# Optimization experiments

Measured on AMD Instinct MI355X. Metric: run time of the kernel, lower is better.

The kernel has to match this reference:

```python
import jax, jax.numpy as jnp
import numpy as np

N = 50000      # nodes
E = 1600000    # edges (avg degree 32)
D_IN = 128
H = 256        # 2 * out_channels
D_OUT = 128
NEG_SLOPE = 0.2


def setup_inputs() -> dict:
    key = jax.random.key(0)
    ks = jax.random.split(key, 16)
    x = jax.random.normal(ks[0], (N, D_IN), dtype=jnp.float32)
    edge_index = jax.random.randint(ks[1], (2, E), 0, N, dtype=jnp.int64)

    def lin(k, fan_in, fan_out):
        s = 1.0 / np.sqrt(fan_in)
        return jax.random.uniform(k, (fan_in, fan_out), jnp.float32, -s, s)

    def att(k, d):
        s = 1.0 / np.sqrt(d)
        return jax.random.uniform(k, (d,), jnp.float32, -s, s)

    return {
        "x": x, "edge_index": edge_index,
        "W1": lin(ks[2], D_IN, H), "a1_src": att(ks[3], H), "a1_dst": att(ks[4], H), "b1": jnp.zeros((H,), jnp.float32),
        "W2": lin(ks[5], H, H),    "a2_src": att(ks[6], H), "a2_dst": att(ks[7], H), "b2": jnp.zeros((H,), jnp.float32),
        "W3": lin(ks[8], H, D_OUT),"a3_src": att(ks[9], D_OUT), "a3_dst": att(ks[10], D_OUT), "b3": jnp.zeros((D_OUT,), jnp.float32),
    }


def _gat_conv(x, W, a_src, a_dst, b, src, dst):
    # x: [N, Cin] -> h: [N, Cout]
    h = x @ W
    # per-node attention logits, gathered along edges (edge j->i: src=j, dst=i)
    e = jax.nn.leaky_relu((h @ a_src)[src] + (h @ a_dst)[dst], NEG_SLOPE)  # [E]
    # segment softmax over incoming edges of each destination node
    m = jax.ops.segment_max(e, dst, num_segments=N)          # [N]
    p = jnp.exp(e - m[dst])                                  # [E]
    denom = jax.ops.segment_sum(p, dst, num_segments=N)      # [N]
    alpha = p / denom[dst]                                   # [E]
    # scatter-add weighted source features
    out = jax.ops.segment_sum(alpha[:, None] * h[src], dst, num_segments=N)
    return out + b


def reference(x, edge_index, W1, a1_src, a1_dst, b1, W2, a2_src, a2_dst, b2, W3, a3_src, a3_dst, b3):
    src, dst = edge_index[0], edge_index[1]
    h = jax.nn.relu(_gat_conv(x, W1, a1_src, a1_dst, b1, src, dst))
    for _ in range(2):  # hidden_layers, shared conv2 weights
        h = jax.nn.relu(_gat_conv(h, W2, a2_src, a2_dst, b2, src, dst))
    out = _gat_conv(h, W3, a3_src, a3_dst, b3, src, dst)
    return jax.nn.softmax(out, axis=1)
```

## Files before the change

kernel.cpp:

```cpp
#include <hip/hip_runtime.h>
#include <hip/hip_bf16.h>
#include <hip/hip_fp16.h>

#define NN 50000
#define EE 1600000
#define DIN 128
#define HH 256
#define DOUT 128

typedef __attribute__((ext_vector_type(8))) short short8;
typedef __attribute__((ext_vector_type(4))) float f32x4;

__device__ __forceinline__ short f2bf(float v) {
    union { float f; unsigned u; } a;
    a.f = v;
    unsigned r = a.u + 0x7fffu + ((a.u >> 16) & 1u);
    return (short)(r >> 16);
}
__device__ __forceinline__ float bf2f(short h) {
    union { unsigned u; float f; } a;
    a.u = ((unsigned)(unsigned short)h) << 16;
    return a.f;
}


__global__ __launch_bounds__(256) void hist_kernel(const int* __restrict__ dst, int* __restrict__ deg, int E) {
    int e = blockIdx.x * 256 + threadIdx.x;
    if (e < E) atomicAdd(&deg[dst[e]], 1);
}

#define SCAN_B 256

__global__ __launch_bounds__(SCAN_B) void scan1_kernel(const int* __restrict__ deg, int* __restrict__ exc,
                                                       int* __restrict__ bsum, int n) {
    __shared__ int tmp[SCAN_B];
    int i = blockIdx.x * SCAN_B + threadIdx.x;
    int v = (i < n) ? deg[i] : 0;
    tmp[threadIdx.x] = v;
    __syncthreads();
    for (int o = 1; o < SCAN_B; o <<= 1) {
        int t = (threadIdx.x >= o) ? tmp[threadIdx.x - o] : 0;
        __syncthreads();
        tmp[threadIdx.x] += t;
        __syncthreads();
    }
    if (i < n) exc[i] = tmp[threadIdx.x] - v;
    if (threadIdx.x == SCAN_B - 1) bsum[blockIdx.x] = tmp[SCAN_B - 1];
}

__global__ __launch_bounds__(SCAN_B) void scan2_kernel(int* __restrict__ bsum, int nb) {
    __shared__ int tmp[SCAN_B];
    int v = (threadIdx.x < nb) ? bsum[threadIdx.x] : 0;
    tmp[threadIdx.x] = v;
    __syncthreads();
    for (int o = 1; o < SCAN_B; o <<= 1) {
        int t = (threadIdx.x >= o) ? tmp[threadIdx.x - o] : 0;
        __syncthreads();
        tmp[threadIdx.x] += t;
        __syncthreads();
    }
    if (threadIdx.x < nb) bsum[threadIdx.x] = tmp[threadIdx.x] - v;
}

__global__ __launch_bounds__(SCAN_B) void scan3_kernel(int* __restrict__ exc, const int* __restrict__ bsum,
                                                       int* __restrict__ cursor, int n, int E) {
    int i = blockIdx.x * SCAN_B + threadIdx.x;
    if (i < n) {
        int v = exc[i] + bsum[blockIdx.x];
        exc[i] = v;
        cursor[i] = v;
    }
    if (i == n) exc[n] = E;
}

__global__ __launch_bounds__(256) void scatter_kernel(const int* __restrict__ src, const int* __restrict__ dst,
                                                      int* __restrict__ cursor, int* __restrict__ es, int E) {
    int e = blockIdx.x * 256 + threadIdx.x;
    if (e < E) {
        int d = dst[e];
        int pos = atomicAdd(&cursor[d], 1);
        es[pos] = src[e];
    }
}


__global__ __launch_bounds__(256) void wsplit_kernel(const float* __restrict__ W, short* __restrict__ WhT,
                                                     short* __restrict__ WlT, int K, int C) {
    int f = blockIdx.x * 256 + threadIdx.x;
    if (f >= K * C) return;
    int k = f / C, c = f % C;
    float v = W[f];
    short h = f2bf(v);
    short l = f2bf(v - bf2f(h));
    WhT[(size_t)c * K + k] = h;
    WlT[(size_t)c * K + k] = l;
}


__global__ __launch_bounds__(256) void tohalf_kernel(const float* __restrict__ in, __half* __restrict__ out,
                                                     size_t cnt) {
    size_t i = (size_t)(blockIdx.x * 256 + threadIdx.x) * 4;
    if (i + 3 < cnt) {
        float4 v = *(const float4*)(in + i);
        __half h0 = __float2half(v.x), h1 = __float2half(v.y);
        __half h2 = __float2half(v.z), h3 = __float2half(v.w);
        __half2* op = (__half2*)(out + i);
        op[0] = __half2(h0, h1);
        op[1] = __half2(h2, h3);
    }
}


template <bool BRELU, bool DOTS, bool HOUT>
__global__ __launch_bounds__(256) void gemm_mfma_kernel(const float* __restrict__ X, const short* __restrict__ BhT,
                                                        const short* __restrict__ BlT, const float* __restrict__ bias,
                                                        float* __restrict__ out, const float* __restrict__ a1v,
                                                        const float* __restrict__ a2v, float* __restrict__ s1,
                                                        float* __restrict__ s2, int n, int K, int Cout) {
    __shared__ short Ah[128][40], Al[128][40];
    __shared__ short Bh[128][40], Bl[128][40];
    int tid = threadIdx.x;
    int row0 = blockIdx.y * 128, col0 = blockIdx.x * 128;
    int lane = tid & 63, wid = tid >> 6;
    int wr = (wid >> 1) * 64, wc = (wid & 1) * 64;

    f32x4 acc[4][4];
#pragma unroll
    for (int mi = 0; mi < 4; ++mi)
#pragma unroll
        for (int ni = 0; ni < 4; ++ni) acc[mi][ni] = 0.f;

    int srow = tid >> 1;
    int sk = (tid & 1) * 16;

    for (int k0 = 0; k0 < K; k0 += 32) {
        {
            float v[16];
            int gr = row0 + srow;
            if (gr < n) {
                const float* p = X + (size_t)gr * K + k0 + sk;
                float4 f0 = ((const float4*)p)[0];
                float4 f1 = ((const float4*)p)[1];
                float4 f2 = ((const float4*)p)[2];
                float4 f3 = ((const float4*)p)[3];
                v[0] = f0.x; v[1] = f0.y; v[2] = f0.z; v[3] = f0.w;
                v[4] = f1.x; v[5] = f1.y; v[6] = f1.z; v[7] = f1.w;
                v[8] = f2.x; v[9] = f2.y; v[10] = f2.z; v[11] = f2.w;
                v[12] = f3.x; v[13] = f3.y; v[14] = f3.z; v[15] = f3.w;
            } else {
#pragma unroll
                for (int j = 0; j < 16; ++j) v[j] = 0.f;
            }
            short8 h0, h1, l0, l1;
#pragma unroll
            for (int j = 0; j < 8; ++j) {
                short h = f2bf(v[j]);
                h0[j] = h;
                l0[j] = f2bf(v[j] - bf2f(h));
            }
#pragma unroll
            for (int j = 0; j < 8; ++j) {
                short h = f2bf(v[8 + j]);
                h1[j] = h;
                l1[j] = f2bf(v[8 + j] - bf2f(h));
            }
            *(short8*)&Ah[srow][sk] = h0;
            *(short8*)&Ah[srow][sk + 8] = h1;
            *(short8*)&Al[srow][sk] = l0;
            *(short8*)&Al[srow][sk + 8] = l1;
        }
        {
            const short* ph = BhT + (size_t)(col0 + srow) * K + k0 + sk;
            const short* pl = BlT + (size_t)(col0 + srow) * K + k0 + sk;
            short8 bh0 = ((const short8*)ph)[0];
            short8 bh1 = ((const short8*)ph)[1];
            short8 bl0 = ((const short8*)pl)[0];
            short8 bl1 = ((const short8*)pl)[1];
            *(short8*)&Bh[srow][sk] = bh0;
            *(short8*)&Bh[srow][sk + 8] = bh1;
            *(short8*)&Bl[srow][sk] = bl0;
            *(short8*)&Bl[srow][sk + 8] = bl1;
        }
        __syncthreads();

        int fr = lane & 15, kb = lane >> 4;
        short8 a_h[4], a_l[4];
#pragma unroll
        for (int mi = 0; mi < 4; ++mi) {
            a_h[mi] = *(const short8*)&Ah[wr + mi * 16 + fr][kb * 8];
            a_l[mi] = *(const short8*)&Al[wr + mi * 16 + fr][kb * 8];
        }
#pragma unroll
        for (int ni = 0; ni < 4; ++ni) {
            short8 b_h = *(const short8*)&Bh[wc + ni * 16 + fr][kb * 8];
            short8 b_l = *(const short8*)&Bl[wc + ni * 16 + fr][kb * 8];
#pragma unroll
            for (int mi = 0; mi < 4; ++mi) {
                acc[mi][ni] = __builtin_amdgcn_mfma_f32_16x16x32_bf16(a_l[mi], b_h, acc[mi][ni], 0, 0, 0);
                acc[mi][ni] = __builtin_amdgcn_mfma_f32_16x16x32_bf16(a_h[mi], b_l, acc[mi][ni], 0, 0, 0);
                acc[mi][ni] = __builtin_amdgcn_mfma_f32_16x16x32_bf16(a_h[mi], b_h, acc[mi][ni], 0, 0, 0);
            }
        }
        __syncthreads();
    }

    int dc = lane & 15, dr = (lane >> 4) * 4;

    if (DOTS) {
#pragma unroll
        for (int mi = 0; mi < 4; ++mi) {
#pragma unroll
            for (int r = 0; r < 4; ++r) {
                float p1 = 0.f, p2 = 0.f;
#pragma unroll
                for (int ni = 0; ni < 4; ++ni) {
                    int gcol = col0 + wc + ni * 16 + dc;
                    float v = acc[mi][ni][r];
                    p1 = fmaf(v, a1v[gcol], p1);
                    p2 = fmaf(v, a2v[gcol], p2);
                }
#pragma unroll
                for (int o = 8; o; o >>= 1) {
                    p1 += __shfl_xor(p1, o, 64);
                    p2 += __shfl_xor(p2, o, 64);
                }
                int grow = row0 + wr + mi * 16 + dr + r;
                if (dc == 0 && grow < n) {
                    atomicAdd(s1 + grow, p1);
                    atomicAdd(s2 + grow, p2);
                }
            }
        }
    }

#pragma unroll
    for (int mi = 0; mi < 4; ++mi) {
#pragma unroll
        for (int r = 0; r < 4; ++r) {
            int grow = row0 + wr + mi * 16 + dr + r;
            if (grow >= n) continue;
#pragma unroll
            for (int ni = 0; ni < 4; ++ni) {
                int gcol = col0 + wc + ni * 16 + dc;
                float v = acc[mi][ni][r];
                if (BRELU) {
                    v += bias[gcol];
                    v = fmaxf(v, 0.f);
                }
                if (HOUT) {
                    ((__half*)out)[(size_t)grow * Cout + gcol] = __float2half(v);
                } else {
                    out[(size_t)grow * Cout + gcol] = v;
                }
            }
        }
    }
}


__global__ __launch_bounds__(256) void rowdots_kernel(const float* __restrict__ H, const float* __restrict__ a1,
                                                      const float* __restrict__ a2, float* __restrict__ s1,
                                                      float* __restrict__ s2, int n, int C) {
    int w = (blockIdx.x * 256 + threadIdx.x) >> 6;
    int lane = threadIdx.x & 63;
    if (w >= n) return;
    const float* hp = H + (size_t)w * C;
    float acc1 = 0.f, acc2 = 0.f;
    for (int c = lane; c < C; c += 64) {
        float hv = hp[c];
        acc1 = fmaf(hv, a1[c], acc1);
        acc2 = fmaf(hv, a2[c], acc2);
    }
#pragma unroll
    for (int o = 32; o; o >>= 1) {
        acc1 += __shfl_xor(acc1, o, 64);
        acc2 += __shfl_xor(acc2, o, 64);
    }
    if (lane == 0) {
        s1[w] = acc1;
        s2[w] = acc2;
    }
}


__global__ __launch_bounds__(256) void mden_kernel(const float* __restrict__ ssrc, const float* __restrict__ sdst,
                                                   const int* __restrict__ off, const int* __restrict__ esrc,
                                                   float* __restrict__ alpha, float* __restrict__ invden, int n) {
    int w = (blockIdx.x * 256 + threadIdx.x) >> 6;
    int lane = threadIdx.x & 63;
    if (w >= n) return;
    int beg = off[w], end = off[w + 1];
    float sd = sdst[w];
    float m = -3e38f;
    for (int e = beg + lane; e < end; e += 64) {
        float v = ssrc[esrc[e]] + sd;
        v = (v > 0.f) ? v : 0.2f * v;
        alpha[e] = v;
        m = fmaxf(m, v);
    }
#pragma unroll
    for (int o = 32; o; o >>= 1) m = fmaxf(m, __shfl_xor(m, o, 64));
    float den = 0.f;
    for (int e = beg + lane; e < end; e += 64) {
        float p = __expf(alpha[e] - m);
        alpha[e] = p;
        den += p;
    }
#pragma unroll
    for (int o = 32; o; o >>= 1) den += __shfl_xor(den, o, 64);
    if (lane == 0) invden[w] = (den > 0.f) ? 1.f / den : 0.f;
}


template <int C, bool RELU, bool SOFTMAX>
__global__ __launch_bounds__(256) void aggc2_kernel(const __half* __restrict__ H, const float* __restrict__ alpha,
                                                    const float* __restrict__ invden, const int* __restrict__ off,
                                                    const int* __restrict__ esrc, const float* __restrict__ bias,
                                                    float* __restrict__ out, int n) {
    constexpr int WPN = C / 128;
    constexpr int NPB = 4 / WPN;
    int wid = threadIdx.x >> 6, lane = threadIdx.x & 63;
    int node = blockIdx.x * NPB + (WPN == 1 ? wid : (wid >> 1));
    int wv = (WPN == 1) ? 0 : (wid & 1);
    int c0 = wv * 128 + lane * 2;
    int beg = (node < n) ? off[node] : 0;
    int end = (node < n) ? off[node + 1] : 0;

    float acc0 = 0.f, acc1 = 0.f;
    for (int base = beg; base < end; base += 64) {
        int e = base + lane;
        float pl = 0.f;
        int sl = 0;
        if (e < end) {
            pl = alpha[e];
            sl = esrc[e];
        }
        int cnt = end - base;
        if (cnt > 64) cnt = 64;
        int j0 = 0;
        for (; j0 + 8 <= cnt; j0 += 8) {
            float pj[8];
            const __half2* hp[8];
#pragma unroll
            for (int u = 0; u < 8; ++u) {
                pj[u] = __shfl(pl, j0 + u, 64);
                int sj = __shfl(sl, j0 + u, 64);
                hp[u] = (const __half2*)(H + (size_t)sj * C + c0);
            }
            __half2 hv[8];
#pragma unroll
            for (int u = 0; u < 8; ++u) hv[u] = *hp[u];
#pragma unroll
            for (int u = 0; u < 8; ++u) {
                float2 f = __half22float2(hv[u]);
                acc0 = fmaf(pj[u], f.x, acc0);
                acc1 = fmaf(pj[u], f.y, acc1);
            }
        }
        for (; j0 < cnt; ++j0) {
            float pj = __shfl(pl, j0, 64);
            int sj = __shfl(sl, j0, 64);
            float2 f = __half22float2(*(const __half2*)(H + (size_t)sj * C + c0));
            acc0 = fmaf(pj, f.x, acc0);
            acc1 = fmaf(pj, f.y, acc1);
        }
    }

    float ov0 = 0.f, ov1 = 0.f;
    if (node < n) {
        float inv = invden[node];
        float bb0 = bias ? bias[c0] : 0.f;
        float bb1 = bias ? bias[c0 + 1] : 0.f;
        ov0 = fmaf(acc0, inv, bb0);
        ov1 = fmaf(acc1, inv, bb1);
        if (RELU) {
            ov0 = fmaxf(ov0, 0.f);
            ov1 = fmaxf(ov1, 0.f);
        }
    }
    if (SOFTMAX) {
        float mm = fmaxf(ov0, ov1);
#pragma unroll
        for (int o = 32; o; o >>= 1) mm = fmaxf(mm, __shfl_xor(mm, o, 64));
        float e0 = __expf(ov0 - mm), e1 = __expf(ov1 - mm);
        float ss = e0 + e1;
#pragma unroll
        for (int o = 32; o; o >>= 1) ss += __shfl_xor(ss, o, 64);
        float si = 1.f / ss;
        ov0 = e0 * si;
        ov1 = e1 * si;
    }
    if (node < n) *(float2*)(out + (size_t)node * C + c0) = make_float2(ov0, ov1);
}


extern "C" void kernel_launch(void* const* d_in, const int* in_sizes, int n_in,
                              void* d_out, int out_size, void* d_ws, size_t ws_size,
                              hipStream_t stream) {
    const float* x = (const float*)d_in[0];
    const int* ei = (const int*)d_in[1];
    const float* W1 = (const float*)d_in[2];
    const float* a1s = (const float*)d_in[3];
    const float* a1d = (const float*)d_in[4];
    const float* b1 = (const float*)d_in[5];
    const float* W2 = (const float*)d_in[6];
    const float* a2s = (const float*)d_in[7];
    const float* a2d = (const float*)d_in[8];
    const float* b2 = (const float*)d_in[9];
    const float* W3 = (const float*)d_in[10];
    const float* a3s = (const float*)d_in[11];
    const float* a3d = (const float*)d_in[12];
    const float* b3 = (const float*)d_in[13];

    const int n = NN, E = EE;
    const int* src = ei;
    const int* dst = ei + E;

    char* base = (char*)d_ws;
    size_t o = 0;
    auto alloc = [&](size_t bytes) -> char* {
        char* p = base + o;
        o += (bytes + 255) & ~(size_t)255;
        return p;
    };
    int* off = (int*)alloc((n + 1) * sizeof(int));
    int* cur = (int*)alloc((n + 1) * sizeof(int));
    int* bsum = (int*)alloc(1024 * sizeof(int));
    int* es = (int*)alloc((size_t)E * sizeof(int));
    float* sbuf = (float*)alloc((size_t)2 * n * sizeof(float));
    float* ssrc = sbuf;
    float* sdst = sbuf + n;
    float* alpha = (float*)alloc((size_t)E * sizeof(float));
    float* invden = (float*)alloc((size_t)n * sizeof(float));
    float* was = (float*)alloc(256 * sizeof(float));
    float* wad = (float*)alloc(256 * sizeof(float));
    short* W1h = (short*)alloc((size_t)DIN * HH * sizeof(short));
    short* W1l = (short*)alloc((size_t)DIN * HH * sizeof(short));
    short* W2h = (short*)alloc((size_t)HH * HH * sizeof(short));
    short* W2l = (short*)alloc((size_t)HH * HH * sizeof(short));
    short* W3h = (short*)alloc((size_t)HH * DOUT * sizeof(short));
    short* W3l = (short*)alloc((size_t)HH * DOUT * sizeof(short));
    __half* xh = (__half*)alloc((size_t)n * DIN * sizeof(__half));
    __half* Hh = (__half*)alloc((size_t)n * HH * sizeof(__half));
    float* Hbuf = (float*)alloc((size_t)n * HH * sizeof(float));
    float* Abuf = (float*)alloc((size_t)n * HH * sizeof(float));
    (void)ws_size;

    hipMemsetAsync(cur, 0, (n + 1) * sizeof(int), stream);
    hist_kernel<<<(E + 255) / 256, 256, 0, stream>>>(dst, cur, E);
    int nb = (n + SCAN_B - 1) / SCAN_B;
    scan1_kernel<<<nb, SCAN_B, 0, stream>>>(cur, off, bsum, n);
    scan2_kernel<<<1, SCAN_B, 0, stream>>>(bsum, nb);
    scan3_kernel<<<nb, SCAN_B, 0, stream>>>(off, bsum, cur, n, E);
    scatter_kernel<<<(E + 255) / 256, 256, 0, stream>>>(src, dst, cur, es, E);

    wsplit_kernel<<<(DIN * HH + 255) / 256, 256, 0, stream>>>(W1, W1h, W1l, DIN, HH);
    wsplit_kernel<<<(HH * HH + 255) / 256, 256, 0, stream>>>(W2, W2h, W2l, HH, HH);
    wsplit_kernel<<<(HH * DOUT + 255) / 256, 256, 0, stream>>>(W3, W3h, W3l, HH, DOUT);
    tohalf_kernel<<<((n * DIN / 4) + 255) / 256, 256, 0, stream>>>(x, xh, (size_t)n * DIN);

    int wgrid = (n * 64 + 255) / 256;
    int rb = (n + 127) / 128;

    {
        rowdots_kernel<<<(128 * 64 + 255) / 256, 256, 0, stream>>>(W1, a1s, a1d, was, wad, DIN, HH);
        rowdots_kernel<<<wgrid, 256, 0, stream>>>(x, was, wad, ssrc, sdst, n, DIN);
        mden_kernel<<<wgrid, 256, 0, stream>>>(ssrc, sdst, off, es, alpha, invden, n);
        aggc2_kernel<DIN, false, false><<<n / 4, 256, 0, stream>>>(xh, alpha, invden, off, es, nullptr, Hbuf, n);
        dim3 g(HH / 128, rb);
        gemm_mfma_kernel<true, false, false><<<g, 256, 0, stream>>>(Hbuf, W1h, W1l, b1, Abuf, nullptr, nullptr,
                                                                    nullptr, nullptr, n, DIN, HH);
    }
    for (int t = 0; t < 2; ++t) {
        dim3 g(HH / 128, rb);
        hipMemsetAsync(sbuf, 0, (size_t)2 * n * sizeof(float), stream);
        gemm_mfma_kernel<false, true, true><<<g, 256, 0, stream>>>(Abuf, W2h, W2l, nullptr, (float*)Hh, a2s, a2d,
                                                                   ssrc, sdst, n, HH, HH);
        mden_kernel<<<wgrid, 256, 0, stream>>>(ssrc, sdst, off, es, alpha, invden, n);
        aggc2_kernel<HH, true, false><<<n / 2, 256, 0, stream>>>(Hh, alpha, invden, off, es, b2, Abuf, n);
    }
    {
        dim3 g(DOUT / 128, rb);
        hipMemsetAsync(sbuf, 0, (size_t)2 * n * sizeof(float), stream);
        gemm_mfma_kernel<false, true, true><<<g, 256, 0, stream>>>(Abuf, W3h, W3l, nullptr, (float*)Hh, a3s, a3d,
                                                                   ssrc, sdst, n, HH, DOUT);
        mden_kernel<<<wgrid, 256, 0, stream>>>(ssrc, sdst, off, es, alpha, invden, n);
        aggc2_kernel<DOUT, false, true><<<n / 4, 256, 0, stream>>>(Hh, alpha, invden, off, es, b3, (float*)d_out, n);
    }
}
```

Measured before the change: 760.7 us.

## Fuse softmax normalization into aggregation and partition CSR scatter by destination range

Removes the separate mden kernel and alpha/invden buffers. The aggregation kernel now recomputes edge logits, takes a per-node max, and computes exp weights and the denominator on the fly while gathering features. It also uses one wave per node with 4 channels per lane for C=256. The CSR scatter is split into 8 destination-range passes over edge chunks to localize atomics and writes, at the cost of reading dst eight times and gathering ssrc twice per edge.

```diff
diff --git a/kernel.cpp b/kernel.cpp
--- a/kernel.cpp
+++ b/kernel.cpp
@@ -73,13 +73,22 @@
     if (i == n) exc[n] = E;
 }
 
-__global__ __launch_bounds__(256) void scatter_kernel(const int* __restrict__ src, const int* __restrict__ dst,
-                                                      int* __restrict__ cursor, int* __restrict__ es, int E) {
-    int e = blockIdx.x * 256 + threadIdx.x;
-    if (e < E) {
+#define NCB 256
+
+__global__ __launch_bounds__(256) void scatter8_kernel(const int* __restrict__ src, const int* __restrict__ dst,
+                                                       int* __restrict__ cursor, int* __restrict__ es, int E, int n) {
+    int q = blockIdx.x & 7;
+    int cb = blockIdx.x >> 3;
+    int lo = q * (n >> 3);
+    int hi = (q == 7) ? n : lo + (n >> 3);
+    int chunk = (E + NCB - 1) / NCB;
+    int e1 = min((cb + 1) * chunk, E);
+    for (int e = cb * chunk + threadIdx.x; e < e1; e += 256) {
         int d = dst[e];
-        int pos = atomicAdd(&cursor[d], 1);
-        es[pos] = src[e];
+        if (d >= lo && d < hi) {
+            int pos = atomicAdd(&cursor[d], 1);
+            es[pos] = src[e];
+        }
     }
 }
 
@@ -283,114 +292,141 @@
 }
 
 
-__global__ __launch_bounds__(256) void mden_kernel(const float* __restrict__ ssrc, const float* __restrict__ sdst,
-                                                   const int* __restrict__ off, const int* __restrict__ esrc,
-                                                   float* __restrict__ alpha, float* __restrict__ invden, int n) {
-    int w = (blockIdx.x * 256 + threadIdx.x) >> 6;
-    int lane = threadIdx.x & 63;
-    if (w >= n) return;
-    int beg = off[w], end = off[w + 1];
-    float sd = sdst[w];
+template <int C, bool RELU, bool SOFTMAX>
+__global__ __launch_bounds__(256) void aggf_kernel(const __half* __restrict__ H, const float* __restrict__ ssrc,
+                                                   const float* __restrict__ sdst, const int* __restrict__ off,
+                                                   const int* __restrict__ es, const float* __restrict__ bias,
+                                                   float* __restrict__ out, int n) {
+    constexpr int VPL = C / 64;
+    int wid = threadIdx.x >> 6, lane = threadIdx.x & 63;
+    int node = blockIdx.x * 4 + wid;
+    if (node >= n) return;
+    int beg = off[node], end = off[node + 1];
+    float sd = sdst[node];
+
     float m = -3e38f;
     for (int e = beg + lane; e < end; e += 64) {
-        float v = ssrc[esrc[e]] + sd;
-        v = (v > 0.f) ? v : 0.2f * v;
-        alpha[e] = v;
-        m = fmaxf(m, v);
+        float g = ssrc[es[e]] + sd;
+        g = (g > 0.f) ? g : 0.2f * g;
+        m = fmaxf(m, g);
     }
 #pragma unroll
     for (int o = 32; o; o >>= 1) m = fmaxf(m, __shfl_xor(m, o, 64));
+
+    float acc[VPL];
+#pragma unroll
+    for (int v = 0; v < VPL; ++v) acc[v] = 0.f;
     float den = 0.f;
-    for (int e = beg + lane; e < end; e += 64) {
-        float p = __expf(alpha[e] - m);
-        alpha[e] = p;
-        den += p;
-    }
-#pragma unroll
-    for (int o = 32; o; o >>= 1) den += __shfl_xor(den, o, 64);
-    if (lane == 0) invden[w] = (den > 0.f) ? 1.f / den : 0.f;
-}
-
-
-template <int C, bool RELU, bool SOFTMAX>
-__global__ __launch_bounds__(256) void aggc2_kernel(const __half* __restrict__ H, const float* __restrict__ alpha,
-                                                    const float* __restrict__ invden, const int* __restrict__ off,
-                                                    const int* __restrict__ esrc, const float* __restrict__ bias,
-                                                    float* __restrict__ out, int n) {
-    constexpr int WPN = C / 128;
-    constexpr int NPB = 4 / WPN;
-    int wid = threadIdx.x >> 6, lane = threadIdx.x & 63;
-    int node = blockIdx.x * NPB + (WPN == 1 ? wid : (wid >> 1));
-    int wv = (WPN == 1) ? 0 : (wid & 1);
-    int c0 = wv * 128 + lane * 2;
-    int beg = (node < n) ? off[node] : 0;
-    int end = (node < n) ? off[node + 1] : 0;
-
-    float acc0 = 0.f, acc1 = 0.f;
+    int c0 = lane * VPL;
+
     for (int base = beg; base < end; base += 64) {
         int e = base + lane;
-        float pl = 0.f;
-        int sl = 0;
+        float p = 0.f;
+        int s = 0;
         if (e < end) {
-            pl = alpha[e];
-            sl = esrc[e];
+            s = es[e];
+            float g = ssrc[s] + sd;
+            g = (g > 0.f) ? g : 0.2f * g;
+            p = __expf(g - m);
+            den += p;
         }
         int cnt = end - base;
         if (cnt > 64) cnt = 64;
         int j0 = 0;
         for (; j0 + 8 <= cnt; j0 += 8) {
             float pj[8];
-            const __half2* hp[8];
+            const __half* hp[8];
 #pragma unroll
             for (int u = 0; u < 8; ++u) {
-                pj[u] = __shfl(pl, j0 + u, 64);
-                int sj = __shfl(sl, j0 + u, 64);
-                hp[u] = (const __half2*)(H + (size_t)sj * C + c0);
-            }
-            __half2 hv[8];
-#pragma unroll
-            for (int u = 0; u < 8; ++u) hv[u] = *hp[u];
-#pragma unroll
-            for (int u = 0; u < 8; ++u) {
-                float2 f = __half22float2(hv[u]);
-                acc0 = fmaf(pj[u], f.x, acc0);
-                acc1 = fmaf(pj[u], f.y, acc1);
+                pj[u] = __shfl(p, j0 + u, 64);
+                int sj = __shfl(s, j0 + u, 64);
+                hp[u] = H + (size_t)sj * C + c0;
+            }
+            if (VPL == 4) {
+                uint2 raw[8];
+#pragma unroll
+                for (int u = 0; u < 8; ++u) raw[u] = *(const uint2*)hp[u];
+#pragma unroll
+                for (int u = 0; u < 8; ++u) {
+                    union { unsigned u32; __half2 h2; } lo, hi;
+                    lo.u32 = raw[u].x;
+                    hi.u32 = raw[u].y;
+                    float2 f0 = __half22float2(lo.h2);
+                    float2 f1 = __half22float2(hi.h2);
+                    acc[0] = fmaf(pj[u], f0.x, acc[0]);
+                    acc[1] = fmaf(pj[u], f0.y, acc[1]);
+                    acc[2] = fmaf(pj[u], f1.x, acc[2]);
+                    acc[3] = fmaf(pj[u], f1.y, acc[3]);
+                }
+            } else {
+                __half2 hv[8];
+#pragma unroll
+                for (int u = 0; u < 8; ++u) hv[u] = *(const __half2*)hp[u];
+#pragma unroll
+                for (int u = 0; u < 8; ++u) {
+                    float2 f = __half22float2(hv[u]);
+                    acc[0] = fmaf(pj[u], f.x, acc[0]);
+                    acc[1] = fmaf(pj[u], f.y, acc[1]);
+                }
             }
         }
         for (; j0 < cnt; ++j0) {
-            float pj = __shfl(pl, j0, 64);
-            int sj = __shfl(sl, j0, 64);
-            float2 f = __half22float2(*(const __half2*)(H + (size_t)sj * C + c0));
-            acc0 = fmaf(pj, f.x, acc0);
-            acc1 = fmaf(pj, f.y, acc1);
-        }
-    }
-
-    float ov0 = 0.f, ov1 = 0.f;
-    if (node < n) {
-        float inv = invden[node];
-        float bb0 = bias ? bias[c0] : 0.f;
-        float bb1 = bias ? bias[c0 + 1] : 0.f;
-        ov0 = fmaf(acc0, inv, bb0);
-        ov1 = fmaf(acc1, inv, bb1);
-        if (RELU) {
-            ov0 = fmaxf(ov0, 0.f);
-            ov1 = fmaxf(ov1, 0.f);
-        }
+            float pj = __shfl(p, j0, 64);
+            int sj = __shfl(s, j0, 64);
+            const __half* hp = H + (size_t)sj * C + c0;
+            if (VPL == 4) {
+                uint2 raw = *(const uint2*)hp;
+                union { unsigned u32; __half2 h2; } lo, hi;
+                lo.u32 = raw.x;
+                hi.u32 = raw.y;
+                float2 f0 = __half22float2(lo.h2);
+                float2 f1 = __half22float2(hi.h2);
+                acc[0] = fmaf(pj, f0.x, acc[0]);
+                acc[1] = fmaf(pj, f0.y, acc[1]);
+                acc[2] = fmaf(pj, f1.x, acc[2]);
+                acc[3] = fmaf(pj, f1.y, acc[3]);
+            } else {
+                float2 f = __half22float2(*(const __half2*)hp);
+                acc[0] = fmaf(pj, f.x, acc[0]);
+                acc[1] = fmaf(pj, f.y, acc[1]);
+            }
+        }
+    }
+
+#pragma unroll
+    for (int o = 32; o; o >>= 1) den += __shfl_xor(den, o, 64);
+    float inv = (den > 0.f) ? 1.f / den : 0.f;
+
+    float ov[VPL];
+#pragma unroll
+    for (int v = 0; v < VPL; ++v) {
+        float bb = bias ? bias[c0 + v] : 0.f;
+        ov[v] = fmaf(acc[v], inv, bb);
+        if (RELU) ov[v] = fmaxf(ov[v], 0.f);
     }
     if (SOFTMAX) {
-        float mm = fmaxf(ov0, ov1);
+        float mm = ov[0];
+#pragma unroll
+        for (int v = 1; v < VPL; ++v) mm = fmaxf(mm, ov[v]);
 #pragma unroll
         for (int o = 32; o; o >>= 1) mm = fmaxf(mm, __shfl_xor(mm, o, 64));
-        float e0 = __expf(ov0 - mm), e1 = __expf(ov1 - mm);
-        float ss = e0 + e1;
+        float ss = 0.f;
+#pragma unroll
+        for (int v = 0; v < VPL; ++v) {
+            ov[v] = __expf(ov[v] - mm);
+            ss += ov[v];
+        }
 #pragma unroll
         for (int o = 32; o; o >>= 1) ss += __shfl_xor(ss, o, 64);
         float si = 1.f / ss;
-        ov0 = e0 * si;
-        ov1 = e1 * si;
-    }
-    if (node < n) *(float2*)(out + (size_t)node * C + c0) = make_float2(ov0, ov1);
+#pragma unroll
+        for (int v = 0; v < VPL; ++v) ov[v] *= si;
+    }
+    float* op = out + (size_t)node * C + c0;
+    if (VPL == 4)
+        *(float4*)op = make_float4(ov[0], ov[1], ov[2], ov[3]);
+    else
+        *(float2*)op = make_float2(ov[0], ov[1]);
 }
 
 
@@ -430,8 +466,6 @@
     float* sbuf = (float*)alloc((size_t)2 * n * sizeof(float));
     float* ssrc = sbuf;
     float* sdst = sbuf + n;
-    float* alpha = (float*)alloc((size_t)E * sizeof(float));
-    float* invden = (float*)alloc((size_t)n * sizeof(float));
     float* was = (float*)alloc(256 * sizeof(float));
     float* wad = (float*)alloc(256 * sizeof(float));
     short* W1h = (short*)alloc((size_t)DIN * HH * sizeof(short));
@@ -452,7 +486,7 @@
     scan1_kernel<<<nb, SCAN_B, 0, stream>>>(cur, off, bsum, n);
     scan2_kernel<<<1, SCAN_B, 0, stream>>>(bsum, nb);
     scan3_kernel<<<nb, SCAN_B, 0, stream>>>(off, bsum, cur, n, E);
-    scatter_kernel<<<(E + 255) / 256, 256, 0, stream>>>(src, dst, cur, es, E);
+    scatter8_kernel<<<NCB * 8, 256, 0, stream>>>(src, dst, cur, es, E, n);
 
     wsplit_kernel<<<(DIN * HH + 255) / 256, 256, 0, stream>>>(W1, W1h, W1l, DIN, HH);
     wsplit_kernel<<<(HH * HH + 255) / 256, 256, 0, stream>>>(W2, W2h, W2l, HH, HH);
@@ -460,13 +494,13 @@
     tohalf_kernel<<<((n * DIN / 4) + 255) / 256, 256, 0, stream>>>(x, xh, (size_t)n * DIN);
 
     int wgrid = (n * 64 + 255) / 256;
+    int agrid = (n + 3) / 4;
     int rb = (n + 127) / 128;
 
     {
         rowdots_kernel<<<(128 * 64 + 255) / 256, 256, 0, stream>>>(W1, a1s, a1d, was, wad, DIN, HH);
         rowdots_kernel<<<wgrid, 256, 0, stream>>>(x, was, wad, ssrc, sdst, n, DIN);
-        mden_kernel<<<wgrid, 256, 0, stream>>>(ssrc, sdst, off, es, alpha, invden, n);
-        aggc2_kernel<DIN, false, false><<<n / 4, 256, 0, stream>>>(xh, alpha, invden, off, es, nullptr, Hbuf, n);
+        aggf_kernel<DIN, false, false><<<agrid, 256, 0, stream>>>(xh, ssrc, sdst, off, es, nullptr, Hbuf, n);
         dim3 g(HH / 128, rb);
         gemm_mfma_kernel<true, false, false><<<g, 256, 0, stream>>>(Hbuf, W1h, W1l, b1, Abuf, nullptr, nullptr,
                                                                     nullptr, nullptr, n, DIN, HH);
@@ -476,15 +510,13 @@
         hipMemsetAsync(sbuf, 0, (size_t)2 * n * sizeof(float), stream);
         gemm_mfma_kernel<false, true, true><<<g, 256, 0, stream>>>(Abuf, W2h, W2l, nullptr, (float*)Hh, a2s, a2d,
                                                                    ssrc, sdst, n, HH, HH);
-        mden_kernel<<<wgrid, 256, 0, stream>>>(ssrc, sdst, off, es, alpha, invden, n);
-        aggc2_kernel<HH, true, false><<<n / 2, 256, 0, stream>>>(Hh, alpha, invden, off, es, b2, Abuf, n);
+        aggf_kernel<HH, true, false><<<agrid, 256, 0, stream>>>(Hh, ssrc, sdst, off, es, b2, Abuf, n);
     }
     {
         dim3 g(DOUT / 128, rb);
         hipMemsetAsync(sbuf, 0, (size_t)2 * n * sizeof(float), stream);
         gemm_mfma_kernel<false, true, true><<<g, 256, 0, stream>>>(Abuf, W3h, W3l, nullptr, (float*)Hh, a3s, a3d,
                                                                    ssrc, sdst, n, HH, DOUT);
-        mden_kernel<<<wgrid, 256, 0, stream>>>(ssrc, sdst, off, es, alpha, invden, n);
-        aggc2_kernel<DOUT, false, true><<<n / 4, 256, 0, stream>>>(Hh, alpha, invden, off, es, b3, (float*)d_out, n);
-    }
-}
+        aggf_kernel<DOUT, false, true><<<agrid, 256, 0, stream>>>(Hh, ssrc, sdst, off, es, b3, (float*)d_out, n);
+    }
+}
```

Result: faster. 665.5 us (-12.5%).
